# Kernel tuning notes

Measured on AMD Instinct MI355X. Metric: run time of the kernel, lower is better.

Reference implementation:

```python
import jax, jax.numpy as jnp
import numpy as np

N, E, IN_DIM, HID, HEADS, L, G, NODES_PER_G = 131072, 524288, 78, 64, 4, 3, 4096, 32
NEG_SLOPE = 0.2


def setup_inputs() -> dict:
    key = jax.random.key(0)
    ks = jax.random.split(key, 20)
    inp = {
        "x": jax.random.normal(ks[0], (N, IN_DIM), jnp.float32),
        "edge_index": jax.random.randint(ks[1], (2, E), 0, N, jnp.int32),
        "batch": (jnp.arange(N, dtype=jnp.int32) // NODES_PER_G),
    }
    dims = [IN_DIM, HID, HID]
    for l in range(L):
        d_in = dims[l]
        inp[f"W{l}"] = jax.random.normal(ks[2 + 4 * l], (d_in, HEADS * HID), jnp.float32) / np.sqrt(d_in)
        inp[f"a_src{l}"] = jax.random.normal(ks[3 + 4 * l], (HEADS, HID), jnp.float32) / np.sqrt(HID)
        inp[f"a_dst{l}"] = jax.random.normal(ks[4 + 4 * l], (HEADS, HID), jnp.float32) / np.sqrt(HID)
        inp[f"b{l}"] = jnp.zeros((HID,), jnp.float32)
    inp["pw"] = jax.random.normal(ks[14], (HID, 1), jnp.float32) / np.sqrt(HID)
    inp["pb"] = jnp.zeros((1,), jnp.float32)
    return inp


def _gat_layer(x, W, a_src, a_dst, b, src, dst):
    # PyG GATConv, concat=False: mean over heads, bias after aggregation.
    h = (x @ W).reshape(N, HEADS, HID)                      # [N,H,D]
    alpha_s = jnp.einsum("nhd,hd->nh", h, a_src)            # [N,H]
    alpha_d = jnp.einsum("nhd,hd->nh", h, a_dst)
    e = jax.nn.leaky_relu(alpha_s[src] + alpha_d[dst], NEG_SLOPE)  # [E',H]
    # scatter-softmax over edges grouped by destination node
    m = jax.ops.segment_max(e, dst, num_segments=N)
    e = jnp.exp(e - m[dst])
    denom = jax.ops.segment_sum(e, dst, num_segments=N)
    alpha = e / denom[dst]                                   # self-loops => denom > 0
    msg = h[src] * alpha[..., None]                          # [E',H,D]
    out = jax.ops.segment_sum(msg, dst, num_segments=N)      # [N,H,D]
    return out.mean(axis=1) + b                              # [N,D]


def reference(x, edge_index, batch, W0, a_src0, a_dst0, b0, W1, a_src1, a_dst1, b1,
              W2, a_src2, a_dst2, b2, pw, pb):
    loop = jnp.arange(N, dtype=edge_index.dtype)
    src = jnp.concatenate([edge_index[0], loop])             # add self loops (PyG default)
    dst = jnp.concatenate([edge_index[1], loop])
    params = [(W0, a_src0, a_dst0, b0), (W1, a_src1, a_dst1, b1), (W2, a_src2, a_dst2, b2)]
    pooled = []
    h = x
    for (W, asr, ads, b) in params:
        h = jax.nn.relu(_gat_layer(h, W, asr, ads, b, src, dst))
        pooled.append(jax.ops.segment_sum(h, batch, num_segments=G))  # global_add_pool
    hstack = jnp.stack(pooled, axis=1)                       # [G,L,D]
    logits = (hstack @ pw).squeeze(-1) + pb                  # [G,L]
    attn = jax.nn.softmax(logits, axis=1)
    return jnp.einsum("gld,gl->gd", hstack, attn)            # [G,D]
```

## Files before the change

kernel.cpp:

```cpp
#include <hip/hip_runtime.h>
#include <math.h>

#define N_NODES 131072
#define N_EDGES 524288
#define IN_DIM_ 78
#define HID_ 64
#define HEADS_ 4
#define NG 4096
#define NPG 32
#define NLAYERS 3
#define NEG_SLOPE 0.2f

typedef __attribute__((ext_vector_type(8))) short bf16x8;
typedef __attribute__((ext_vector_type(4))) float f32x4;

__device__ __forceinline__ unsigned short f2bf(float f) {
    unsigned int u = __float_as_uint(f);
    u = (u + 0x7FFF + ((u >> 16) & 1)) >> 16;
    return (unsigned short)u;
}
__device__ __forceinline__ float bf2f(unsigned short u) {
    return __uint_as_float(((unsigned int)u) << 16);
}


__global__ void init_counts(int* __restrict__ cnt) {
    int n = blockIdx.x * blockDim.x + threadIdx.x;
    if (n < N_NODES) cnt[n] = 1;
}

__global__ void count_edges(const int* __restrict__ dst, int* __restrict__ cnt) {
    int e = blockIdx.x * blockDim.x + threadIdx.x;
    if (e < N_EDGES) atomicAdd(&cnt[dst[e]], 1);
}

__global__ void scan_kernel(const int* __restrict__ cnt, int* __restrict__ offsets) {
    __shared__ int sums[1024];
    const int t = threadIdx.x;
    const int CHUNK = N_NODES / 1024;
    int base = t * CHUNK;
    int s = 0;
    for (int j = 0; j < CHUNK / 4; ++j) {
        int4 v = ((const int4*)(cnt + base))[j];
        s += v.x + v.y + v.z + v.w;
    }
    sums[t] = s;
    __syncthreads();
    for (int off = 1; off < 1024; off <<= 1) {
        int v = (t >= off) ? sums[t - off] : 0;
        __syncthreads();
        sums[t] += v;
        __syncthreads();
    }
    int run = (t == 0) ? 0 : sums[t - 1];
    for (int j = 0; j < CHUNK / 4; ++j) {
        int4 c = ((const int4*)(cnt + base))[j];
        int4 o;
        o.x = run; run += c.x;
        o.y = run; run += c.y;
        o.z = run; run += c.z;
        o.w = run; run += c.w;
        ((int4*)(offsets + base))[j] = o;
    }
    if (t == 1023) offsets[N_NODES] = run;
}

__global__ void place_self(const int* __restrict__ offsets, int* __restrict__ cursor,
                           int* __restrict__ csr_src) {
    int n = blockIdx.x * blockDim.x + threadIdx.x;
    if (n < N_NODES) {
        int o = offsets[n];
        csr_src[o] = n;
        cursor[n] = o + 1;
    }
}

__global__ void scatter_edges(const int* __restrict__ src, const int* __restrict__ dst,
                              int* __restrict__ cursor, int* __restrict__ csr_src) {
    int e = blockIdx.x * blockDim.x + threadIdx.x;
    if (e < N_EDGES) {
        int d = dst[e];
        int pos = atomicAdd(&cursor[d], 1);
        csr_src[pos] = src[e];
    }
}

__global__ void wsplit(const float* __restrict__ W, int K,
                       unsigned short* __restrict__ WtH, unsigned short* __restrict__ WtL) {
    int k = blockIdx.x;
    int col = threadIdx.x;
    float w = (k < K) ? W[k * 256 + col] : 0.f;
    unsigned short hi = f2bf(w);
    unsigned short lo = f2bf(w - bf2f(hi));
    WtH[col * 96 + k] = hi;
    WtL[col * 96 + k] = lo;
}

template<int NCH, int K>
__global__ __launch_bounds__(256, 3)
void gemm_mfma(const float* __restrict__ A,
               const unsigned short* __restrict__ WtH,
               const unsigned short* __restrict__ WtL,
               const float* __restrict__ a_src, const float* __restrict__ a_dst,
               unsigned short* __restrict__ h, float* __restrict__ als, float* __restrict__ ald) {
    constexpr int AS = 104;
    constexpr int BS = 40;
    constexpr int KP = NCH * 32;
    __shared__ __align__(16) unsigned short AsH[64 * AS];
    __shared__ __align__(16) unsigned short AsL[64 * AS];
    __shared__ __align__(16) unsigned short Bst[256 * BS];
    const int tid = threadIdx.x;
    const int w = tid >> 6;
    const int lane = tid & 63;
    const int li = lane & 15, lg = lane >> 4;
    const int row0 = blockIdx.x * 64;
    const int r0 = (w >> 1) * 32, c0 = (w & 1) * 128;

    {
        const float2* Ab = (const float2*)(A + (size_t)row0 * K);
        constexpr int NF2 = 64 * K / 2;
        for (int i = tid; i < NF2; i += 256) {
            float2 v = Ab[i];
            int row = (2 * i) / K, k = (2 * i) % K;
            unsigned short hx = f2bf(v.x);
            unsigned short lx = f2bf(v.x - bf2f(hx));
            unsigned short hy = f2bf(v.y);
            unsigned short ly = f2bf(v.y - bf2f(hy));
            ushort2 hv; hv.x = hx; hv.y = hy;
            ushort2 lv; lv.x = lx; lv.y = ly;
            *(ushort2*)&AsH[row * AS + k] = hv;
            *(ushort2*)&AsL[row * AS + k] = lv;
        }
        if constexpr (KP > K) {
            constexpr int PAD2 = (KP - K) / 2;
            for (int i = tid; i < 64 * PAD2; i += 256) {
                int row = i / PAD2, j = i - row * PAD2;
                int k = K + 2 * j;
                *(unsigned int*)&AsH[row * AS + k] = 0u;
                *(unsigned int*)&AsL[row * AS + k] = 0u;
            }
        }
    }

    ushort4 breg[8];
    auto loadB = [&](const unsigned short* __restrict__ Wt, int ch) {
        #pragma unroll
        for (int m = 0; m < 8; ++m) {
            int idx = m * 256 + tid;
            int col = idx >> 3, k4 = idx & 7;
            breg[m] = *(const ushort4*)&Wt[col * 96 + ch * 32 + k4 * 4];
        }
    };
    auto writeB = [&]() {
        #pragma unroll
        for (int m = 0; m < 8; ++m) {
            int idx = m * 256 + tid;
            int col = idx >> 3, k4 = idx & 7;
            *(ushort4*)&Bst[col * BS + k4 * 4] = breg[m];
        }
    };

    f32x4 acc[2][8];
    #pragma unroll
    for (int rt = 0; rt < 2; ++rt)
        #pragma unroll
        for (int ct = 0; ct < 8; ++ct)
            acc[rt][ct] = (f32x4){0.f, 0.f, 0.f, 0.f};

    loadB(WtH, 0);
    writeB();
    __syncthreads();

    #pragma unroll
    for (int ch = 0; ch < NCH; ++ch) {
        bf16x8 ah[2], al[2];
        #pragma unroll
        for (int rt = 0; rt < 2; ++rt) {
            int aoff = (r0 + rt * 16 + li) * AS + ch * 32 + lg * 8;
            ah[rt] = *(const bf16x8*)&AsH[aoff];
            al[rt] = *(const bf16x8*)&AsL[aoff];
        }
        loadB(WtL, ch);
        #pragma unroll
        for (int ct = 0; ct < 8; ++ct) {
            bf16x8 bh = *(const bf16x8*)&Bst[(c0 + ct * 16 + li) * BS + lg * 8];
            #pragma unroll
            for (int rt = 0; rt < 2; ++rt) {
                acc[rt][ct] = __builtin_amdgcn_mfma_f32_16x16x32_bf16(ah[rt], bh, acc[rt][ct], 0, 0, 0);
                acc[rt][ct] = __builtin_amdgcn_mfma_f32_16x16x32_bf16(al[rt], bh, acc[rt][ct], 0, 0, 0);
            }
        }
        __syncthreads();
        writeB();
        __syncthreads();
        if (ch + 1 < NCH) loadB(WtH, ch + 1);
        #pragma unroll
        for (int ct = 0; ct < 8; ++ct) {
            bf16x8 bl = *(const bf16x8*)&Bst[(c0 + ct * 16 + li) * BS + lg * 8];
            #pragma unroll
            for (int rt = 0; rt < 2; ++rt)
                acc[rt][ct] = __builtin_amdgcn_mfma_f32_16x16x32_bf16(ah[rt], bl, acc[rt][ct], 0, 0, 0);
        }
        if (ch + 1 < NCH) {
            __syncthreads();
            writeB();
            __syncthreads();
        }
    }

    #pragma unroll
    for (int rt = 0; rt < 2; ++rt) {
        #pragma unroll
        for (int ct = 0; ct < 8; ++ct) {
            #pragma unroll
            for (int reg = 0; reg < 4; ++reg) {
                int row = row0 + r0 + rt * 16 + lg * 4 + reg;
                int col = c0 + ct * 16 + li;
                unsigned int v = f2bf(acc[rt][ct][reg]);
                unsigned int pv = (unsigned int)__shfl_xor((int)v, 1, 64) & 0xFFFFu;
                if ((li & 1) == 0)
                    *(unsigned int*)&h[(size_t)row * 256 + col] = v | (pv << 16);
            }
        }
    }

    float as_v[8], ad_v[8];
    #pragma unroll
    for (int ct = 0; ct < 8; ++ct) {
        int ghead = (w & 1) * 2 + (ct >> 2);
        as_v[ct] = a_src[ghead * 64 + (ct & 3) * 16 + li];
        ad_v[ct] = a_dst[ghead * 64 + (ct & 3) * 16 + li];
    }
    #pragma unroll
    for (int rt = 0; rt < 2; ++rt) {
        #pragma unroll
        for (int hl = 0; hl < 2; ++hl) {
            #pragma unroll
            for (int reg = 0; reg < 4; ++reg) {
                float ps = 0.f, pd = 0.f;
                #pragma unroll
                for (int c4 = 0; c4 < 4; ++c4) {
                    int ct = hl * 4 + c4;
                    ps += acc[rt][ct][reg] * as_v[ct];
                    pd += acc[rt][ct][reg] * ad_v[ct];
                }
                ps += __shfl_xor(ps, 1, 64); ps += __shfl_xor(ps, 2, 64);
                ps += __shfl_xor(ps, 4, 64); ps += __shfl_xor(ps, 8, 64);
                pd += __shfl_xor(pd, 1, 64); pd += __shfl_xor(pd, 2, 64);
                pd += __shfl_xor(pd, 4, 64); pd += __shfl_xor(pd, 8, 64);
                if (li == 0) {
                    int row = row0 + r0 + rt * 16 + lg * 4 + reg;
                    int ghead = (w & 1) * 2 + hl;
                    als[row * 4 + ghead] = ps;
                    ald[row * 4 + ghead] = pd;
                }
            }
        }
    }
}

__device__ __forceinline__ float pick4(float4 v, int idx) {
    float r = v.x;
    r = (idx == 1) ? v.y : r;
    r = (idx == 2) ? v.z : r;
    r = (idx == 3) ? v.w : r;
    return r;
}

__global__ __launch_bounds__(256)
void aggregate(const int* __restrict__ offsets, const int* __restrict__ csr_src,
               const unsigned short* __restrict__ h, const float* __restrict__ als,
               const float* __restrict__ ald, const float* __restrict__ bias,
               float* __restrict__ hout) {
    const int lane = threadIdx.x & 63;
    const int wid = __builtin_amdgcn_readfirstlane(threadIdx.x >> 6);
    const int n = blockIdx.x * 4 + wid;
    const int head = lane >> 4;
    const int d4 = (lane & 15) * 4;

    const int o0 = __builtin_amdgcn_readfirstlane(offsets[n]);
    const int o1 = __builtin_amdgcn_readfirstlane(offsets[n + 1]);

    const float ad_h = pick4(*(const float4*)&ald[n * 4], head);

    float4 acc = make_float4(0.f, 0.f, 0.f, 0.f);
    float den = 0.f;

    int i = o0;
    for (; i + 4 <= o1; i += 4) {
        int s0 = __builtin_amdgcn_readfirstlane(csr_src[i + 0]);
        int s1 = __builtin_amdgcn_readfirstlane(csr_src[i + 1]);
        int s2 = __builtin_amdgcn_readfirstlane(csr_src[i + 2]);
        int s3 = __builtin_amdgcn_readfirstlane(csr_src[i + 3]);
        float4 as0 = *(const float4*)&als[s0 * 4];
        float4 as1 = *(const float4*)&als[s1 * 4];
        float4 as2 = *(const float4*)&als[s2 * 4];
        float4 as3 = *(const float4*)&als[s3 * 4];
        ushort4 u0 = ((const ushort4*)(h + (size_t)s0 * 256))[lane];
        ushort4 u1 = ((const ushort4*)(h + (size_t)s1 * 256))[lane];
        ushort4 u2 = ((const ushort4*)(h + (size_t)s2 * 256))[lane];
        ushort4 u3 = ((const ushort4*)(h + (size_t)s3 * 256))[lane];
        float e0 = pick4(as0, head) + ad_h; e0 = e0 > 0.f ? e0 : NEG_SLOPE * e0;
        float e1 = pick4(as1, head) + ad_h; e1 = e1 > 0.f ? e1 : NEG_SLOPE * e1;
        float e2 = pick4(as2, head) + ad_h; e2 = e2 > 0.f ? e2 : NEG_SLOPE * e2;
        float e3 = pick4(as3, head) + ad_h; e3 = e3 > 0.f ? e3 : NEG_SLOPE * e3;
        float p0 = __expf(e0), p1 = __expf(e1), p2 = __expf(e2), p3 = __expf(e3);
        den += p0 + p1 + p2 + p3;
        acc.x += p0 * bf2f(u0.x) + p1 * bf2f(u1.x) + p2 * bf2f(u2.x) + p3 * bf2f(u3.x);
        acc.y += p0 * bf2f(u0.y) + p1 * bf2f(u1.y) + p2 * bf2f(u2.y) + p3 * bf2f(u3.y);
        acc.z += p0 * bf2f(u0.z) + p1 * bf2f(u1.z) + p2 * bf2f(u2.z) + p3 * bf2f(u3.z);
        acc.w += p0 * bf2f(u0.w) + p1 * bf2f(u1.w) + p2 * bf2f(u2.w) + p3 * bf2f(u3.w);
    }
    for (; i < o1; ++i) {
        int s = __builtin_amdgcn_readfirstlane(csr_src[i]);
        float4 asv = *(const float4*)&als[s * 4];
        ushort4 uv = ((const ushort4*)(h + (size_t)s * 256))[lane];
        float e = pick4(asv, head) + ad_h;
        e = e > 0.f ? e : NEG_SLOPE * e;
        float p = __expf(e);
        den += p;
        acc.x += p * bf2f(uv.x); acc.y += p * bf2f(uv.y);
        acc.z += p * bf2f(uv.z); acc.w += p * bf2f(uv.w);
    }

    const float rden = 1.f / den;
    float c0 = acc.x * rden, c1 = acc.y * rden, c2 = acc.z * rden, c3 = acc.w * rden;
    c0 += __shfl_xor(c0, 16, 64); c0 += __shfl_xor(c0, 32, 64);
    c1 += __shfl_xor(c1, 16, 64); c1 += __shfl_xor(c1, 32, 64);
    c2 += __shfl_xor(c2, 16, 64); c2 += __shfl_xor(c2, 32, 64);
    c3 += __shfl_xor(c3, 16, 64); c3 += __shfl_xor(c3, 32, 64);

    if (lane < 16) {
        float4 bv = *(const float4*)&bias[d4];
        float v0 = 0.25f * c0 + bv.x;
        float v1 = 0.25f * c1 + bv.y;
        float v2 = 0.25f * c2 + bv.z;
        float v3 = 0.25f * c3 + bv.w;
        float4 o;
        o.x = v0 > 0.f ? v0 : 0.f;
        o.y = v1 > 0.f ? v1 : 0.f;
        o.z = v2 > 0.f ? v2 : 0.f;
        o.w = v3 > 0.f ? v3 : 0.f;
        *(float4*)&hout[(size_t)n * 64 + d4] = o;
    }
}

__global__ __launch_bounds__(256)
void pool_kernel(const float* __restrict__ hout, float* __restrict__ pooled, int layer) {
    const int wid = threadIdx.x >> 6, lane = threadIdx.x & 63;
    const int g = blockIdx.x * 4 + wid;
    float s = 0.f;
    const float* p = &hout[(size_t)g * NPG * 64 + lane];
    #pragma unroll 8
    for (int i = 0; i < NPG; ++i) s += p[i * 64];
    pooled[(g * NLAYERS + layer) * 64 + lane] = s;
}

__global__ __launch_bounds__(256)
void final_kernel(const float* __restrict__ pooled, const float* __restrict__ pw,
                  const float* __restrict__ pb, float* __restrict__ out) {
    const int wid = threadIdx.x >> 6, lane = threadIdx.x & 63;
    const int g = blockIdx.x * 4 + wid;
    float v0 = pooled[(g * 3 + 0) * 64 + lane];
    float v1 = pooled[(g * 3 + 1) * 64 + lane];
    float v2 = pooled[(g * 3 + 2) * 64 + lane];
    float w = pw[lane];
    float l0 = v0 * w, l1 = v1 * w, l2 = v2 * w;
    #pragma unroll
    for (int m = 1; m < 64; m <<= 1) {
        l0 += __shfl_xor(l0, m, 64);
        l1 += __shfl_xor(l1, m, 64);
        l2 += __shfl_xor(l2, m, 64);
    }
    float bb = pb[0];
    l0 += bb; l1 += bb; l2 += bb;
    float mx = fmaxf(l0, fmaxf(l1, l2));
    float e0 = __expf(l0 - mx), e1 = __expf(l1 - mx), e2 = __expf(l2 - mx);
    float inv = 1.f / (e0 + e1 + e2);
    out[(size_t)g * 64 + lane] = (v0 * e0 + v1 * e1 + v2 * e2) * inv;
}

extern "C" void kernel_launch(void* const* d_in, const int* in_sizes, int n_in,
                              void* d_out, int out_size, void* d_ws, size_t ws_size,
                              hipStream_t stream) {
    const float* x  = (const float*)d_in[0];
    const int*   ei = (const int*)d_in[1];
    const float* W[3]    = {(const float*)d_in[3], (const float*)d_in[7],  (const float*)d_in[11]};
    const float* asrc[3] = {(const float*)d_in[4], (const float*)d_in[8],  (const float*)d_in[12]};
    const float* adst[3] = {(const float*)d_in[5], (const float*)d_in[9],  (const float*)d_in[13]};
    const float* bias[3] = {(const float*)d_in[6], (const float*)d_in[10], (const float*)d_in[14]};
    const float* pw = (const float*)d_in[15];
    const float* pb = (const float*)d_in[16];
    float* out = (float*)d_out;

    char* ws = (char*)d_ws;
    size_t off = 0;
    auto alloc = [&](size_t bytes) -> void* {
        void* p = ws + off;
        off = (off + bytes + 255) & ~(size_t)255;
        return p;
    };
    int*   offsets = (int*)alloc((N_NODES + 1) * 4);
    int*   cursor  = (int*)alloc(N_NODES * 4);
    int*   csr_src = (int*)alloc((size_t)(N_EDGES + N_NODES) * 4);
    unsigned short* h = (unsigned short*)alloc((size_t)N_NODES * 256 * 2);
    float* als     = (float*)alloc((size_t)N_NODES * 4 * 4);
    float* ald     = (float*)alloc((size_t)N_NODES * 4 * 4);
    float* hbuf0   = (float*)alloc((size_t)N_NODES * 64 * 4);
    float* hbuf1   = (float*)alloc((size_t)N_NODES * 64 * 4);
    float* pooled  = (float*)alloc((size_t)NG * 3 * 64 * 4);
    unsigned short* WtH = (unsigned short*)alloc((size_t)256 * 96 * 2);
    unsigned short* WtL = (unsigned short*)alloc((size_t)256 * 96 * 2);
    (void)ws_size; (void)in_sizes; (void)n_in; (void)out_size;

    const int* srcp = ei;
    const int* dstp = ei + N_EDGES;

    init_counts<<<N_NODES / 256, 256, 0, stream>>>(cursor);
    count_edges<<<N_EDGES / 256, 256, 0, stream>>>(dstp, cursor);
    scan_kernel<<<1, 1024, 0, stream>>>(cursor, offsets);
    place_self<<<N_NODES / 256, 256, 0, stream>>>(offsets, cursor, csr_src);
    scatter_edges<<<N_EDGES / 256, 256, 0, stream>>>(srcp, dstp, cursor, csr_src);

    const float* in = x;
    for (int l = 0; l < 3; ++l) {
        const int K = (l == 0) ? IN_DIM_ : HID_;
        wsplit<<<96, 256, 0, stream>>>(W[l], K, WtH, WtL);
        if (l == 0)
            gemm_mfma<3, IN_DIM_><<<N_NODES / 64, 256, 0, stream>>>(in, WtH, WtL, asrc[l], adst[l], h, als, ald);
        else
            gemm_mfma<2, HID_><<<N_NODES / 64, 256, 0, stream>>>(in, WtH, WtL, asrc[l], adst[l], h, als, ald);
        float* ho = (l & 1) ? hbuf1 : hbuf0;
        aggregate<<<N_NODES / 4, 256, 0, stream>>>(offsets, csr_src, h, als, ald, bias[l], ho);
        pool_kernel<<<NG / 4, 256, 0, stream>>>(ho, pooled, l);
        in = ho;
    }
    final_kernel<<<NG / 4, 256, 0, stream>>>(pooled, pw, pb, out);
}
```

Before: 570.1 us.

## Load GEMM A and B fragments straight into registers, dropping LDS staging

The MFMA GEMM no longer stages A (split into bf16 hi/lo) and W fragments through shared memory. Each lane now loads its A fragment directly from global memory and splits it in registers, and reads B fragments directly from the pre-transposed weight buffers, which removes all __syncthreads barriers. The goal is to cut LDS traffic and barrier stalls. In exchange, register use goes up (launch bounds drop from 3 to 2 blocks per SM), B is read redundantly from global/L2 by every wave, and the A loads are less coalesced.

```diff
diff --git a/kernel.cpp b/kernel.cpp
--- a/kernel.cpp
+++ b/kernel.cpp
@@ -97,18 +97,12 @@
 }
 
 template<int NCH, int K>
-__global__ __launch_bounds__(256, 3)
+__global__ __launch_bounds__(256, 2)
 void gemm_mfma(const float* __restrict__ A,
                const unsigned short* __restrict__ WtH,
                const unsigned short* __restrict__ WtL,
                const float* __restrict__ a_src, const float* __restrict__ a_dst,
                unsigned short* __restrict__ h, float* __restrict__ als, float* __restrict__ ald) {
-    constexpr int AS = 104;
-    constexpr int BS = 40;
-    constexpr int KP = NCH * 32;
-    __shared__ __align__(16) unsigned short AsH[64 * AS];
-    __shared__ __align__(16) unsigned short AsL[64 * AS];
-    __shared__ __align__(16) unsigned short Bst[256 * BS];
     const int tid = threadIdx.x;
     const int w = tid >> 6;
     const int lane = tid & 63;
@@ -116,49 +110,46 @@
     const int row0 = blockIdx.x * 64;
     const int r0 = (w >> 1) * 32, c0 = (w & 1) * 128;
 
-    {
-        const float2* Ab = (const float2*)(A + (size_t)row0 * K);
-        constexpr int NF2 = 64 * K / 2;
-        for (int i = tid; i < NF2; i += 256) {
-            float2 v = Ab[i];
-            int row = (2 * i) / K, k = (2 * i) % K;
-            unsigned short hx = f2bf(v.x);
-            unsigned short lx = f2bf(v.x - bf2f(hx));
-            unsigned short hy = f2bf(v.y);
-            unsigned short ly = f2bf(v.y - bf2f(hy));
-            ushort2 hv; hv.x = hx; hv.y = hy;
-            ushort2 lv; lv.x = lx; lv.y = ly;
-            *(ushort2*)&AsH[row * AS + k] = hv;
-            *(ushort2*)&AsL[row * AS + k] = lv;
+    bf16x8 ah[NCH][2], al[NCH][2];
+    #pragma unroll
+    for (int ch = 0; ch < NCH; ++ch) {
+        #pragma unroll
+        for (int rt = 0; rt < 2; ++rt) {
+            const int row = row0 + r0 + rt * 16 + li;
+            const int kb = ch * 32 + lg * 8;
+            float t[8];
+            if ((ch + 1) * 32 <= K) {
+                if constexpr ((K % 4) == 0) {
+                    const float4* ap = (const float4*)(A + (size_t)row * K + kb);
+                    float4 v0 = ap[0], v1 = ap[1];
+                    t[0] = v0.x; t[1] = v0.y; t[2] = v0.z; t[3] = v0.w;
+                    t[4] = v1.x; t[5] = v1.y; t[6] = v1.z; t[7] = v1.w;
+                } else {
+                    const float2* ap = (const float2*)(A + (size_t)row * K + kb);
+                    #pragma unroll
+                    for (int j = 0; j < 4; ++j) {
+                        float2 v = ap[j];
+                        t[2 * j] = v.x; t[2 * j + 1] = v.y;
+                    }
+                }
+            } else {
+                const float2* ap = (const float2*)(A + (size_t)row * K + kb);
+                #pragma unroll
+                for (int j = 0; j < 4; ++j) {
+                    float2 v = (kb + 2 * j + 1 < K) ? ap[j] : make_float2(0.f, 0.f);
+                    t[2 * j] = v.x; t[2 * j + 1] = v.y;
+                }
+            }
+            bf16x8 hh, ll;
+            #pragma unroll
+            for (int j = 0; j < 8; ++j) {
+                unsigned short hi = f2bf(t[j]);
+                unsigned short lo = f2bf(t[j] - bf2f(hi));
+                hh[j] = (short)hi; ll[j] = (short)lo;
+            }
+            ah[ch][rt] = hh; al[ch][rt] = ll;
         }
-        if constexpr (KP > K) {
-            constexpr int PAD2 = (KP - K) / 2;
-            for (int i = tid; i < 64 * PAD2; i += 256) {
-                int row = i / PAD2, j = i - row * PAD2;
-                int k = K + 2 * j;
-                *(unsigned int*)&AsH[row * AS + k] = 0u;
-                *(unsigned int*)&AsL[row * AS + k] = 0u;
-            }
-        }
-    }
-
-    ushort4 breg[8];
-    auto loadB = [&](const unsigned short* __restrict__ Wt, int ch) {
-        #pragma unroll
-        for (int m = 0; m < 8; ++m) {
-            int idx = m * 256 + tid;
-            int col = idx >> 3, k4 = idx & 7;
-            breg[m] = *(const ushort4*)&Wt[col * 96 + ch * 32 + k4 * 4];
-        }
-    };
-    auto writeB = [&]() {
-        #pragma unroll
-        for (int m = 0; m < 8; ++m) {
-            int idx = m * 256 + tid;
-            int col = idx >> 3, k4 = idx & 7;
-            *(ushort4*)&Bst[col * BS + k4 * 4] = breg[m];
-        }
-    };
+    }
 
     f32x4 acc[2][8];
     #pragma unroll
@@ -167,44 +158,19 @@
         for (int ct = 0; ct < 8; ++ct)
             acc[rt][ct] = (f32x4){0.f, 0.f, 0.f, 0.f};
 
-    loadB(WtH, 0);
-    writeB();
-    __syncthreads();
-
     #pragma unroll
     for (int ch = 0; ch < NCH; ++ch) {
-        bf16x8 ah[2], al[2];
-        #pragma unroll
-        for (int rt = 0; rt < 2; ++rt) {
-            int aoff = (r0 + rt * 16 + li) * AS + ch * 32 + lg * 8;
-            ah[rt] = *(const bf16x8*)&AsH[aoff];
-            al[rt] = *(const bf16x8*)&AsL[aoff];
-        }
-        loadB(WtL, ch);
         #pragma unroll
         for (int ct = 0; ct < 8; ++ct) {
-            bf16x8 bh = *(const bf16x8*)&Bst[(c0 + ct * 16 + li) * BS + lg * 8];
-            #pragma unroll
-            for (int rt = 0; rt < 2; ++rt) {
-                acc[rt][ct] = __builtin_amdgcn_mfma_f32_16x16x32_bf16(ah[rt], bh, acc[rt][ct], 0, 0, 0);
-                acc[rt][ct] = __builtin_amdgcn_mfma_f32_16x16x32_bf16(al[rt], bh, acc[rt][ct], 0, 0, 0);
-            }
-        }
-        __syncthreads();
-        writeB();
-        __syncthreads();
-        if (ch + 1 < NCH) loadB(WtH, ch + 1);
-        #pragma unroll
-        for (int ct = 0; ct < 8; ++ct) {
-            bf16x8 bl = *(const bf16x8*)&Bst[(c0 + ct * 16 + li) * BS + lg * 8];
-            #pragma unroll
-            for (int rt = 0; rt < 2; ++rt)
-                acc[rt][ct] = __builtin_amdgcn_mfma_f32_16x16x32_bf16(ah[rt], bl, acc[rt][ct], 0, 0, 0);
-        }
-        if (ch + 1 < NCH) {
-            __syncthreads();
-            writeB();
-            __syncthreads();
+            const size_t boff = (size_t)(c0 + ct * 16 + li) * 96 + ch * 32 + lg * 8;
+            bf16x8 bh = *(const bf16x8*)&WtH[boff];
+            bf16x8 bl = *(const bf16x8*)&WtL[boff];
+            acc[0][ct] = __builtin_amdgcn_mfma_f32_16x16x32_bf16(ah[ch][0], bh, acc[0][ct], 0, 0, 0);
+            acc[1][ct] = __builtin_amdgcn_mfma_f32_16x16x32_bf16(ah[ch][1], bh, acc[1][ct], 0, 0, 0);
+            acc[0][ct] = __builtin_amdgcn_mfma_f32_16x16x32_bf16(al[ch][0], bh, acc[0][ct], 0, 0, 0);
+            acc[1][ct] = __builtin_amdgcn_mfma_f32_16x16x32_bf16(al[ch][1], bh, acc[1][ct], 0, 0, 0);
+            acc[0][ct] = __builtin_amdgcn_mfma_f32_16x16x32_bf16(ah[ch][0], bl, acc[0][ct], 0, 0, 0);
+            acc[1][ct] = __builtin_amdgcn_mfma_f32_16x16x32_bf16(ah[ch][1], bl, acc[1][ct], 0, 0, 0);
         }
     }
 
```

Measured after the change: 591.2 us. 3.7% more time.
